# Kernel tuning notes

Hardware: AMD Instinct MI355X
Metric: run time of the kernel (lower is better)

The kernel has to match this reference:

```python
import jax, jax.numpy as jnp
import numpy as np

N = 16384  # number of internal DAG nodes
L = 16384  # number of leaves


def setup_inputs() -> dict:
    key = jax.random.key(0)
    ks = jax.random.split(key, 12)
    idx = jnp.arange(N)
    # internal-child offsets and leaf ids
    off_l = jax.random.randint(ks[0], (N,), 1, N)
    off_r = jax.random.randint(ks[1], (N,), 1, N)
    leaf_l = jax.random.randint(ks[2], (N,), 0, L)
    leaf_r = jax.random.randint(ks[3], (N,), 0, L)
    is_int_l = (jax.random.uniform(ks[4], (N,)) < 0.5) & (idx < N - 1)
    is_int_r = (jax.random.uniform(ks[5], (N,)) < 0.5) & (idx < N - 1)
    # forward-pointing DAG: internal child index strictly greater than parent
    left = jnp.where(is_int_l, jnp.clip(idx + off_l, 0, N - 1), -(leaf_l + 1)).astype(jnp.int32)
    right = jnp.where(is_int_r, jnp.clip(idx + off_r, 0, N - 1), -(leaf_r + 1)).astype(jnp.int32)
    return {
        "thresholds": jax.random.normal(ks[6], (N,), dtype=jnp.float32),
        "rules": jax.random.randint(ks[7], (N,), 0, 16).astype(jnp.int32),
        "binary_ops": jax.random.randint(ks[8], (N,), 0, 8).astype(jnp.int32),
        "left": left,
        "right": right,
        "leaf_is_reroll": jax.random.uniform(ks[9], (L,)) < 0.5,
        "leaf_mask_left": jax.random.randint(ks[10], (L,), 0, 64).astype(jnp.int32),
        "leaf_mask_right": jax.random.randint(ks[11], (L,), 0, 64).astype(jnp.int32),
        "leaf_mask_op": jax.random.randint(jax.random.fold_in(key, 100), (L,), 0, 4).astype(jnp.int32),
        "leaf_score_cat": jax.random.randint(jax.random.fold_in(key, 101), (L,), 0, 16).astype(jnp.int32),
    }


def _active_mask(left, right, n_nodes):
    def step(reachable, _):
        active_left = jnp.where(reachable & (left >= 0), left, n_nodes)
        active_right = jnp.where(reachable & (right >= 0), right, n_nodes)
        new_reachable = jnp.zeros(n_nodes + 1, dtype=jnp.bool_)
        new_reachable = new_reachable.at[active_left].set(True)
        new_reachable = new_reachable.at[active_right].set(True)
        new_reachable = new_reachable.at[0].set(True)
        return new_reachable[:n_nodes] | reachable, None

    init = jnp.zeros(n_nodes, dtype=jnp.bool_).at[0].set(True)
    mask, _ = jax.lax.scan(step, init, None, length=n_nodes)
    return mask


def _subtree_leaf_flags(left, right, leaf_is_reroll, n):
    def is_leaf_score(child):
        leaf_id = -child - 1
        return (child < 0) & (~leaf_is_reroll[leaf_id])

    def is_leaf_reroll(child):
        leaf_id = -child - 1
        return (child < 0) & leaf_is_reroll[leaf_id]

    def step(carry, i):
        has_score, has_reroll = carry
        node = n - 1 - i  # postorder: children have larger indices
        l, r = left[node], right[node]

        def child_has_score(child):
            return is_leaf_score(child) | jnp.where(child >= 0, has_score[child], False)

        def child_has_reroll(child):
            return is_leaf_reroll(child) | jnp.where(child >= 0, has_reroll[child], False)

        has_score = has_score.at[node].set(child_has_score(l) | child_has_score(r))
        has_reroll = has_reroll.at[node].set(child_has_reroll(l) | child_has_reroll(r))
        return (has_score, has_reroll), None

    init = (jnp.zeros(n, dtype=jnp.bool_), jnp.zeros(n, dtype=jnp.bool_))
    (has_score, has_reroll), _ = jax.lax.scan(step, init, jnp.arange(n))
    return has_score, has_reroll


def reference(thresholds, rules, binary_ops, left, right, leaf_is_reroll,
              leaf_mask_left, leaf_mask_right, leaf_mask_op, leaf_score_cat):
    n = rules.shape[0]
    active_mask = _active_mask(left, right, n)
    has_score, has_reroll = _subtree_leaf_flags(left, right, leaf_is_reroll, n)
    active_node_count = jnp.sum(active_mask)
    return active_mask, has_score, has_reroll, active_node_count
```

## Files before the change

kernel.cpp:

```cpp
#include <hip/hip_runtime.h>

#define NN 16384
#define NT 1024

__global__ __launch_bounds__(NT) void dag_eval_kernel(
    const int* __restrict__ left,
    const int* __restrict__ right,
    const unsigned char* __restrict__ reroll_raw,
    int* __restrict__ out)
{
    __shared__ __align__(16) unsigned char reach[NN];
    __shared__ __align__(16) unsigned char state[NN + 16];
    __shared__ int flags[4];
    __shared__ int nzmask;
    __shared__ int cnt;

    const int tid = threadIdx.x;

    if (tid < 4)  flags[tid] = 0;
    if (tid == 0) { nzmask = 0; cnt = 0; }
    if (tid < 16) state[NN + tid] = 4;

    unsigned int cpair[16];
    #pragma unroll
    for (int k = 0; k < 16; ++k) {
        int l = left[tid + k * NT];
        int r = right[tid + k * NT];
        cpair[k] = (l & 0xFFFFu) | ((unsigned)r << 16);
    }

    {
        uint4 v = ((const uint4*)reroll_raw)[tid];
        unsigned int t = v.x | v.y | v.z | v.w;
        unsigned int m = 0;
        if (t & 0x000000FFu) m |= 1u;
        if (t & 0x0000FF00u) m |= 2u;
        if (t & 0x00FF0000u) m |= 4u;
        if (t & 0xFF000000u) m |= 8u;
        if (m) atomicOr(&nzmask, (int)m);
    }
    *(uint4*)&reach[tid * 16] = make_uint4(0u, 0u, 0u, 0u);
    __syncthreads();

    const int mask   = nzmask;
    const int layout = ((mask & ~1) == 0) ? 0 : (((mask & 3) == 0) ? 1 : 2);
    const int*   ri = (const int*)reroll_raw;
    const float* rf = (const float*)reroll_raw;

    int sreg[16];
    unsigned int todo = 0;
    #pragma unroll
    for (int k = 0; k < 16; ++k) {
        int c0 = (int)(short)(cpair[k] & 0xFFFFu);
        int c1 = (int)(short)(cpair[k] >> 16);
        int s = 0;
        if (c0 < 0) {
            int id = -c0 - 1;
            bool rr = (layout == 2) ? (reroll_raw[id] != 0)
                     : (layout == 1) ? (rf[id] != 0.0f)
                                     : (ri[id] != 0);
            s |= rr ? 2 : 1;
        }
        if (c1 < 0) {
            int id = -c1 - 1;
            bool rr = (layout == 2) ? (reroll_raw[id] != 0)
                     : (layout == 1) ? (rf[id] != 0.0f)
                                     : (ri[id] != 0);
            s |= rr ? 2 : 1;
        }
        if ((c0 < 0 && c1 < 0) || s == 3) s |= 4;
        else todo |= 1u << k;
        sreg[k] = s;
        state[tid + k * NT] = (unsigned char)s;
    }
    if (tid == 0) reach[0] = 1;
    __syncthreads();

    unsigned int pushed = 0;
    for (int w = 0; w < 600; ++w) {
        bool ch = false;

        #pragma unroll
        for (int kp = 0; kp < 8; ++kp) {
            const int k0 = 2 * kp, k1 = 2 * kp + 1;
            unsigned int need = (~pushed >> k0) & 3u;
            if (need) {
                int r0 = (need & 1u) ? (int)reach[tid + k0 * NT] : 0;
                int r1 = (need & 2u) ? (int)reach[tid + k1 * NT] : 0;
                if (r0) {
                    pushed |= 1u << k0; ch = true;
                    int c0 = (int)(short)(cpair[k0] & 0xFFFFu);
                    int c1 = (int)(short)(cpair[k0] >> 16);
                    if (c0 > 0) reach[c0] = (unsigned char)1;
                    if (c1 > 0) reach[c1] = (unsigned char)1;
                }
                if (r1) {
                    pushed |= 1u << k1; ch = true;
                    int c0 = (int)(short)(cpair[k1] & 0xFFFFu);
                    int c1 = (int)(short)(cpair[k1] >> 16);
                    if (c0 > 0) reach[c0] = (unsigned char)1;
                    if (c1 > 0) reach[c1] = (unsigned char)1;
                }
            }
        }

        if (todo) {
            #pragma unroll
            for (int kp = 7; kp >= 0; --kp) {
                const int k0 = 2 * kp, k1 = 2 * kp + 1;
                if ((todo >> k0) & 3u) {
                    bool a1 = (todo >> k1) & 1u;
                    bool a0 = (todo >> k0) & 1u;
                    int c10 = (int)(short)(cpair[k1] & 0xFFFFu);
                    int c11 = (int)(short)(cpair[k1] >> 16);
                    int c00 = (int)(short)(cpair[k0] & 0xFFFFu);
                    int c01 = (int)(short)(cpair[k0] >> 16);
                    int sl1 = state[(a1 && c10 > 0) ? c10 : NN];
                    int sr1 = state[(a1 && c11 > 0) ? c11 : NN];
                    int sl0 = state[(a0 && c00 > 0) ? c00 : NN];
                    int sr0 = state[(a0 && c01 > 0) ? c01 : NN];
                    if (a1) {
                        int ns = sreg[k1] | (sl1 & 3) | (sr1 & 3);
                        bool fin = ((sl1 & sr1 & 4) != 0) || ((ns & 3) == 3);
                        if (fin) { ns |= 4; todo &= ~(1u << k1); }
                        if (ns != sreg[k1]) {
                            sreg[k1] = ns;
                            state[tid + k1 * NT] = (unsigned char)ns;
                            ch = true;
                        }
                    }
                    if (a0) {
                        int ns = sreg[k0] | (sl0 & 3) | (sr0 & 3);
                        bool fin = ((sl0 & sr0 & 4) != 0) || ((ns & 3) == 3);
                        if (fin) { ns |= 4; todo &= ~(1u << k0); }
                        if (ns != sreg[k0]) {
                            sreg[k0] = ns;
                            state[tid + k0 * NT] = (unsigned char)ns;
                            ch = true;
                        }
                    }
                }
            }
        }

        if (ch) flags[w & 3] = 1;
        __syncthreads();
        int f = flags[w & 3];
        if (tid == 0) flags[(w + 2) & 3] = 0;
        if (!f) break;
    }

    uint4 v = *(const uint4*)&reach[tid * 16];
    {
        unsigned int t = v.x + v.y + v.z + v.w;
        int cc = (t & 0xFF) + ((t >> 8) & 0xFF) + ((t >> 16) & 0xFF) + (t >> 24);
        #pragma unroll
        for (int off = 32; off; off >>= 1) cc += __shfl_down(cc, off);
        if ((tid & 63) == 0) atomicAdd(&cnt, cc);
    }

    int4* out4 = (int4*)out;
    {
        unsigned int wd[4] = {v.x, v.y, v.z, v.w};
        #pragma unroll
        for (int j = 0; j < 4; ++j) {
            int4 a;
            a.x = (wd[j] >> 0)  & 1;
            a.y = (wd[j] >> 8)  & 1;
            a.z = (wd[j] >> 16) & 1;
            a.w = (wd[j] >> 24) & 1;
            out4[(tid * 16 >> 2) + j] = a;
        }
    }
    {
        uint4 sv = *(const uint4*)&state[tid * 16];
        unsigned int wd[4] = {sv.x, sv.y, sv.z, sv.w};
        #pragma unroll
        for (int j = 0; j < 4; ++j) {
            int4 h, r;
            h.x = (wd[j] >> 0)  & 1; h.y = (wd[j] >> 8)  & 1;
            h.z = (wd[j] >> 16) & 1; h.w = (wd[j] >> 24) & 1;
            r.x = (wd[j] >> 1)  & 1; r.y = (wd[j] >> 9)  & 1;
            r.z = (wd[j] >> 17) & 1; r.w = (wd[j] >> 25) & 1;
            out4[((NN + tid * 16) >> 2) + j]     = h;
            out4[((2 * NN + tid * 16) >> 2) + j] = r;
        }
    }
    __syncthreads();
    if (tid == 0) out[3 * NN] = cnt;
}

extern "C" void kernel_launch(void* const* d_in, const int* in_sizes, int n_in,
                              void* d_out, int out_size, void* d_ws, size_t ws_size,
                              hipStream_t stream)
{
    const int* left  = (const int*)d_in[3];
    const int* right = (const int*)d_in[4];
    const unsigned char* reroll = (const unsigned char*)d_in[5];
    int* out = (int*)d_out;
    dag_eval_kernel<<<1, NT, 0, stream>>>(left, right, reroll, out);
}
```

Measured before the change: 36.30 us.

## Add ordered chunk sweep prologue and per-child pending tracking for DAG flags

Adds a 16-step prologue that walks the node chunks in order, propagating reachability forward and subtree flags backward with a barrier after each chunk, so most nodes settle before the iterative fixed-point loop starts. Per-child pending bits let finished children be skipped instead of gathering both children every sweep. The main loop now gathers reach bits for all chunks before pushing. It adds a shared pairs array that is written but never read, and 16 extra barriers, in exchange for fewer fixed-point iterations.

New measurement: 38.18 us. +5.2%, slower.

```diff
diff --git a/kernel.cpp b/kernel.cpp
--- a/kernel.cpp
+++ b/kernel.cpp
@@ -2,6 +2,31 @@
 
 #define NN 16384
 #define NT 1024
+
+#define BWD_GATHER(K)                                                        \
+    {                                                                        \
+        unsigned int p2 = (pend >> (2 * (K))) & 3u;                          \
+        int ns = sreg[(K)];                                                  \
+        if (p2 & 1u) {                                                       \
+            int c0 = (int)(short)(cpair[(K)] & 0xFFFFu);                     \
+            int s = state[c0];                                               \
+            ns |= s & 3;                                                     \
+            if (s & 4) p2 &= ~1u;                                            \
+        }                                                                    \
+        if (p2 & 2u) {                                                       \
+            int c1 = (int)(short)(cpair[(K)] >> 16);                         \
+            int s = state[c1];                                               \
+            ns |= s & 3;                                                     \
+            if (s & 4) p2 &= ~2u;                                            \
+        }                                                                    \
+        if (p2 == 0u || (ns & 3) == 3) { ns |= 4; todo &= ~(1u << (K)); }    \
+        pend = (pend & ~(3u << (2 * (K)))) | (p2 << (2 * (K)));              \
+        if (ns != sreg[(K)]) {                                               \
+            sreg[(K)] = ns;                                                  \
+            state[((K) << 10) + tid] = (unsigned char)ns;                    \
+            ch = true;                                                       \
+        }                                                                    \
+    }
 
 __global__ __launch_bounds__(NT) void dag_eval_kernel(
     const int* __restrict__ left,
@@ -9,8 +34,9 @@
     const unsigned char* __restrict__ reroll_raw,
     int* __restrict__ out)
 {
+    __shared__ __align__(16) unsigned int  pairs[NN];
     __shared__ __align__(16) unsigned char reach[NN];
-    __shared__ __align__(16) unsigned char state[NN + 16];
+    __shared__ __align__(16) unsigned char state[NN];
     __shared__ int flags[4];
     __shared__ int nzmask;
     __shared__ int cnt;
@@ -19,14 +45,14 @@
 
     if (tid < 4)  flags[tid] = 0;
     if (tid == 0) { nzmask = 0; cnt = 0; }
-    if (tid < 16) state[NN + tid] = 4;
 
     unsigned int cpair[16];
     #pragma unroll
     for (int k = 0; k < 16; ++k) {
-        int l = left[tid + k * NT];
-        int r = right[tid + k * NT];
+        int l = left[(k << 10) + tid];
+        int r = right[(k << 10) + tid];
         cpair[k] = (l & 0xFFFFu) | ((unsigned)r << 16);
+        pairs[(k << 10) + tid] = cpair[k];
     }
 
     {
@@ -48,56 +74,71 @@
     const float* rf = (const float*)reroll_raw;
 
     int sreg[16];
-    unsigned int todo = 0;
+    unsigned int todo = 0, pend = 0;
     #pragma unroll
     for (int k = 0; k < 16; ++k) {
         int c0 = (int)(short)(cpair[k] & 0xFFFFu);
         int c1 = (int)(short)(cpair[k] >> 16);
         int s = 0;
+        unsigned int p2 = 0;
         if (c0 < 0) {
             int id = -c0 - 1;
             bool rr = (layout == 2) ? (reroll_raw[id] != 0)
                      : (layout == 1) ? (rf[id] != 0.0f)
                                      : (ri[id] != 0);
             s |= rr ? 2 : 1;
-        }
+        } else p2 |= 1u;
         if (c1 < 0) {
             int id = -c1 - 1;
             bool rr = (layout == 2) ? (reroll_raw[id] != 0)
                      : (layout == 1) ? (rf[id] != 0.0f)
                                      : (ri[id] != 0);
             s |= rr ? 2 : 1;
-        }
-        if ((c0 < 0 && c1 < 0) || s == 3) s |= 4;
-        else todo |= 1u << k;
+        } else p2 |= 2u;
+        if (p2 == 0u || s == 3) s |= 4;
+        else { todo |= 1u << k; pend |= p2 << (2 * k); }
         sreg[k] = s;
-        state[tid + k * NT] = (unsigned char)s;
+        state[(k << 10) + tid] = (unsigned char)s;
     }
     if (tid == 0) reach[0] = 1;
     __syncthreads();
 
-    unsigned int pushed = 0;
+    unsigned int pushedC = 0;
+    #pragma unroll
+    for (int c = 0; c < 16; ++c) {
+        {
+            if (reach[(c << 10) + tid]) {
+                pushedC |= 1u << c;
+                int c0 = (int)(short)(cpair[c] & 0xFFFFu);
+                int c1 = (int)(short)(cpair[c] >> 16);
+                if (c0 > 0) reach[c0] = (unsigned char)1;
+                if (c1 > 0) reach[c1] = (unsigned char)1;
+            }
+        }
+        {
+            bool ch = false;
+            if ((todo >> (15 - c)) & 1u) BWD_GATHER(15 - c);
+            if ((todo >> (15 - c)) & 1u) BWD_GATHER(15 - c);
+            (void)ch;
+        }
+        __syncthreads();
+    }
+
     for (int w = 0; w < 600; ++w) {
         bool ch = false;
 
-        #pragma unroll
-        for (int kp = 0; kp < 8; ++kp) {
-            const int k0 = 2 * kp, k1 = 2 * kp + 1;
-            unsigned int need = (~pushed >> k0) & 3u;
-            if (need) {
-                int r0 = (need & 1u) ? (int)reach[tid + k0 * NT] : 0;
-                int r1 = (need & 2u) ? (int)reach[tid + k1 * NT] : 0;
-                if (r0) {
-                    pushed |= 1u << k0; ch = true;
-                    int c0 = (int)(short)(cpair[k0] & 0xFFFFu);
-                    int c1 = (int)(short)(cpair[k0] >> 16);
-                    if (c0 > 0) reach[c0] = (unsigned char)1;
-                    if (c1 > 0) reach[c1] = (unsigned char)1;
-                }
-                if (r1) {
-                    pushed |= 1u << k1; ch = true;
-                    int c0 = (int)(short)(cpair[k1] & 0xFFFFu);
-                    int c1 = (int)(short)(cpair[k1] >> 16);
+        unsigned int np = 0;
+        #pragma unroll
+        for (int k = 0; k < 16; ++k)
+            if (!((pushedC >> k) & 1u) && reach[(k << 10) + tid]) np |= 1u << k;
+        if (np) {
+            pushedC |= np;
+            ch = true;
+            #pragma unroll
+            for (int k = 0; k < 16; ++k) {
+                if ((np >> k) & 1u) {
+                    int c0 = (int)(short)(cpair[k] & 0xFFFFu);
+                    int c1 = (int)(short)(cpair[k] >> 16);
                     if (c0 > 0) reach[c0] = (unsigned char)1;
                     if (c1 > 0) reach[c1] = (unsigned char)1;
                 }
@@ -106,41 +147,8 @@
 
         if (todo) {
             #pragma unroll
-            for (int kp = 7; kp >= 0; --kp) {
-                const int k0 = 2 * kp, k1 = 2 * kp + 1;
-                if ((todo >> k0) & 3u) {
-                    bool a1 = (todo >> k1) & 1u;
-                    bool a0 = (todo >> k0) & 1u;
-                    int c10 = (int)(short)(cpair[k1] & 0xFFFFu);
-                    int c11 = (int)(short)(cpair[k1] >> 16);
-                    int c00 = (int)(short)(cpair[k0] & 0xFFFFu);
-                    int c01 = (int)(short)(cpair[k0] >> 16);
-                    int sl1 = state[(a1 && c10 > 0) ? c10 : NN];
-                    int sr1 = state[(a1 && c11 > 0) ? c11 : NN];
-                    int sl0 = state[(a0 && c00 > 0) ? c00 : NN];
-                    int sr0 = state[(a0 && c01 > 0) ? c01 : NN];
-                    if (a1) {
-                        int ns = sreg[k1] | (sl1 & 3) | (sr1 & 3);
-                        bool fin = ((sl1 & sr1 & 4) != 0) || ((ns & 3) == 3);
-                        if (fin) { ns |= 4; todo &= ~(1u << k1); }
-                        if (ns != sreg[k1]) {
-                            sreg[k1] = ns;
-                            state[tid + k1 * NT] = (unsigned char)ns;
-                            ch = true;
-                        }
-                    }
-                    if (a0) {
-                        int ns = sreg[k0] | (sl0 & 3) | (sr0 & 3);
-                        bool fin = ((sl0 & sr0 & 4) != 0) || ((ns & 3) == 3);
-                        if (fin) { ns |= 4; todo &= ~(1u << k0); }
-                        if (ns != sreg[k0]) {
-                            sreg[k0] = ns;
-                            state[tid + k0 * NT] = (unsigned char)ns;
-                            ch = true;
-                        }
-                    }
-                }
-            }
+            for (int k = 0; k < 16; ++k)
+                if ((todo >> k) & 1u) BWD_GATHER(k);
         }
 
         if (ch) flags[w & 3] = 1;
```
